# Optimization experiments

Measured on AMD Instinct MI355X. Metric: run time of the kernel, lower is better.

Reference implementation:

```python
import jax, jax.numpy as jnp
import numpy as np

GDEP = 3
BETA = 0.05
C_IN = 32
C_OUT = 64
N_NODES = 512
B = 8
SEQ = 256


def setup_inputs() -> dict:
    key = jax.random.key(0)
    k1, k2, k3, k4 = jax.random.split(key, 4)
    X = jax.random.normal(k1, (B, C_IN, N_NODES, SEQ), dtype=jnp.float32)
    A = jax.random.uniform(k2, (N_NODES, N_NODES), dtype=jnp.float32)
    # 1x1 conv over channels: weight [c_out, (gdep+1)*c_in], bias [c_out]
    fan_in = (GDEP + 1) * C_IN
    limit = float(np.sqrt(6.0 / (C_OUT + fan_in)))  # xavier_uniform
    W = jax.random.uniform(k3, (C_OUT, fan_in), minval=-limit, maxval=limit, dtype=jnp.float32)
    b = jax.random.uniform(k4, (C_OUT,), dtype=jnp.float32)
    return {"X": X, "A": A, "W": W, "b": b}


def reference(X, A, W, b):
    # A <- row-normalized (A + I)
    n = A.shape[0]
    A = A + jnp.eye(n, dtype=A.dtype)
    A = A / jnp.sum(A, axis=1, keepdims=True)
    H = X
    hops = [X]
    for _ in range(GDEP):
        # Hk[n,c,v,l] = sum_w H[n,c,w,l] * A[v,w]
        Hk = jnp.einsum('ncwl,vw->ncvl', H, A)
        H = BETA * X + (1.0 - BETA) * Hk
        hops.append(H)
    H0 = jnp.concatenate(hops, axis=1)  # [B, (gdep+1)*c_in, N, L]
    # 1x1 conv == channel matmul
    out = jnp.einsum('bcnl,oc->bonl', H0, W) + b[None, :, None, None]
    return out
```

## Files before the change

kernel.cpp:

```cpp
#include <hip/hip_runtime.h>


#define NODES 512
#define SEQL  256
#define CIN   32
#define COUT  64
#define NB    8
#define PLANE (NODES * SEQL)
#define BETA_F 0.05f

typedef _Float16 f16x8 __attribute__((ext_vector_type(8)));
typedef _Float16 f16x2 __attribute__((ext_vector_type(2)));
typedef float    f32x4 __attribute__((ext_vector_type(4)));

typedef const unsigned int __attribute__((address_space(1)))* gptr_t;
typedef unsigned int __attribute__((address_space(3)))* lptr_t;

__device__ __forceinline__ void gload16(const void* g, void* l) {
    __builtin_amdgcn_global_load_lds((gptr_t)g, (lptr_t)l, 16, 0, 0);
}

__device__ __forceinline__ unsigned short f2h(float f) {
    _Float16 h = (_Float16)f;
    return __builtin_bit_cast(unsigned short, h);
}

__global__ __launch_bounds__(256) void norm_A_kernel(const float* __restrict__ A,
                                                     _Float16* __restrict__ Apb) {
    const int v = blockIdx.x;
    const int t = threadIdx.x;
    __shared__ float red[256];
    float s = 0.f;
    for (int w = t; w < NODES; w += 256)
        s += A[v * NODES + w] + (w == v ? 1.f : 0.f);
    red[t] = s;
    __syncthreads();
    for (int off = 128; off > 0; off >>= 1) {
        if (t < off) red[t] += red[t + off];
        __syncthreads();
    }
    const float inv = (1.f - BETA_F) / red[0];
    for (int w = t; w < NODES; w += 256) {
        const float a = A[v * NODES + w] + (w == v ? 1.f : 0.f);
        Apb[v * NODES + w] = (_Float16)(a * inv);
    }
}

__global__ __launch_bounds__(256) void prep_W_kernel(const float* __restrict__ W,
                                                     float* __restrict__ Wt,
                                                     unsigned int* __restrict__ Wp) {
    const int i = blockIdx.x * 256 + threadIdx.x;
    const int o = i >> 7, c = i & 127;
    Wt[c * COUT + o] = W[i];
    if (i < 4096) {
        const int p = i >> 6, oo = i & 63;
        Wp[i] = (unsigned)f2h(W[oo * 128 + 2 * p]) |
                ((unsigned)f2h(W[oo * 128 + 2 * p + 1]) << 16);
    }
}

__global__ __launch_bounds__(256) void prep_X_kernel(const float* __restrict__ X,
                                                     unsigned short* __restrict__ Xt) {
    const int l0 = blockIdx.x * 64, v0 = blockIdx.y * 64;
    const size_t coff = (size_t)blockIdx.z * PLANE;
    __shared__ unsigned short t[64][66];
    const int rr = threadIdx.x >> 4;
    const int cc = (threadIdx.x & 15) * 4;
#pragma unroll
    for (int rep = 0; rep < 4; ++rep) {
        const int vl = rep * 16 + rr;
        const float4 f = *(const float4*)(X + coff + (size_t)(v0 + vl) * SEQL + l0 + cc);
        t[cc + 0][vl] = f2h(f.x);
        t[cc + 1][vl] = f2h(f.y);
        t[cc + 2][vl] = f2h(f.z);
        t[cc + 3][vl] = f2h(f.w);
    }
    __syncthreads();
#pragma unroll
    for (int rep = 0; rep < 4; ++rep) {
        const int ll = rep * 16 + rr;
        ushort4 d;
        d.x = t[ll][cc + 0]; d.y = t[ll][cc + 1];
        d.z = t[ll][cc + 2]; d.w = t[ll][cc + 3];
        *(ushort4*)(Xt + coff + (size_t)(l0 + ll) * NODES + v0 + cc) = d;
    }
}

__global__ __launch_bounds__(256) void transpose_h_kernel(const unsigned short* __restrict__ src,
                                                          unsigned short* __restrict__ dst) {
    const int v0 = blockIdx.x * 64, l0 = blockIdx.y * 64;
    const size_t coff = (size_t)blockIdx.z * PLANE;
    __shared__ unsigned short t[64][66];
    const int rr = threadIdx.x >> 4;
    const int cc = (threadIdx.x & 15) * 4;
#pragma unroll
    for (int rep = 0; rep < 4; ++rep) {
        const int ll = rep * 16 + rr;
        const ushort4 s = *(const ushort4*)(src + coff + (size_t)(l0 + ll) * NODES + v0 + cc);
        t[cc + 0][ll] = s.x; t[cc + 1][ll] = s.y;
        t[cc + 2][ll] = s.z; t[cc + 3][ll] = s.w;
    }
    __syncthreads();
#pragma unroll
    for (int rep = 0; rep < 4; ++rep) {
        const int vl = rep * 16 + rr;
        ushort4 d;
        d.x = t[vl][cc + 0]; d.y = t[vl][cc + 1];
        d.z = t[vl][cc + 2]; d.w = t[vl][cc + 3];
        *(ushort4*)(dst + coff + (size_t)(v0 + vl) * SEQL + l0 + cc) = d;
    }
}

__global__ __launch_bounds__(256) void prop_mfma_kernel(
    const _Float16* __restrict__ Apb,
    const _Float16* __restrict__ Hin,
    const _Float16* __restrict__ Xt,
    _Float16* __restrict__ Hout)
{
    __shared__ _Float16 Asl[128 * 64];
    __shared__ _Float16 Bsl[128 * 64];

    const int tid  = threadIdx.x;
    const int wave = tid >> 6;
    const int lane = tid & 63;
    const int n0 = blockIdx.x * 128;
    const int m0 = blockIdx.y * 128;
    const size_t coff = (size_t)blockIdx.z * PLANE;
    const _Float16* Asrc = Hin + coff;

    const int wm = (wave >> 1) * 64;
    const int wn = (wave & 1) * 64;
    const int lane15 = lane & 15;
    const int quad = lane >> 4;
    const int srow = lane >> 3;
    const int spos = lane & 7;

    f32x4 acc[4][4] = {};

    for (int kk = 0; kk < 8; ++kk) {
        const int k0 = kk * 64;
#pragma unroll
        for (int j = 0; j < 4; ++j) {
            const int r = wave * 32 + j * 8 + srow;
            const int gc = k0 + ((spos ^ (r & 7)) << 3);
            gload16(Asrc + (size_t)(m0 + r) * NODES + gc, &Asl[(wave * 32 + j * 8) * 64]);
            gload16(Apb  + (size_t)(n0 + r) * NODES + gc, &Bsl[(wave * 32 + j * 8) * 64]);
        }
        __syncthreads();
#pragma unroll
        for (int ks = 0; ks < 2; ++ks) {
            f16x8 af[4], bf[4];
#pragma unroll
            for (int mt = 0; mt < 4; ++mt) {
                const int m = wm + mt * 16 + lane15;
                const int pos = (ks * 4 + quad) ^ (m & 7);
                af[mt] = *(const f16x8*)&Asl[m * 64 + pos * 8];
            }
#pragma unroll
            for (int nt = 0; nt < 4; ++nt) {
                const int n = wn + nt * 16 + lane15;
                const int pos = (ks * 4 + quad) ^ (n & 7);
                bf[nt] = *(const f16x8*)&Bsl[n * 64 + pos * 8];
            }
#pragma unroll
            for (int mt = 0; mt < 4; ++mt)
#pragma unroll
                for (int nt = 0; nt < 4; ++nt)
                    acc[mt][nt] = __builtin_amdgcn_mfma_f32_16x16x32_f16(
                        af[mt], bf[nt], acc[mt][nt], 0, 0, 0);
        }
        __syncthreads();
    }

#pragma unroll
    for (int mt = 0; mt < 4; ++mt) {
#pragma unroll
        for (int nt = 0; nt < 4; ++nt) {
            const int l = m0 + wm + mt * 16 + quad * 4;
            const int v = n0 + wn + nt * 16 + lane15;
            const size_t base = coff + (size_t)l * NODES + v;
#pragma unroll
            for (int r = 0; r < 4; ++r) {
                const size_t a = base + (size_t)r * NODES;
                Hout[a] = (_Float16)(acc[mt][nt][r] + BETA_F * (float)Xt[a]);
            }
        }
    }
}

__global__ __launch_bounds__(256) void final_kernel(
    const float* __restrict__ X,
    const _Float16* __restrict__ H1,
    const _Float16* __restrict__ H2,
    const _Float16* __restrict__ H3,
    const float* __restrict__ Wt,
    const unsigned int* __restrict__ Wp,
    const float* __restrict__ bias,
    float* __restrict__ out)
{
    const int v = blockIdx.x, b = blockIdx.y, l = threadIdx.x;
    const size_t vl = (size_t)v * SEQL + l;

    float acc[COUT];
#pragma unroll
    for (int o = 0; o < COUT; ++o) acc[o] = bias[o];

    {
        const float* P = X + (size_t)b * CIN * PLANE + vl;
        for (int c = 0; c < CIN; ++c) {
            const float x = P[(size_t)c * PLANE];
            const float* wr = Wt + c * COUT;
#pragma unroll
            for (int o = 0; o < COUT; ++o) acc[o] += wr[o] * x;
        }
    }
    const _Float16* Hs[3] = {H1, H2, H3};
#pragma unroll
    for (int g = 0; g < 3; ++g) {
        const _Float16* P = Hs[g] + (size_t)b * CIN * PLANE + vl;
        for (int cp = 0; cp < 16; ++cp) {
            const _Float16 h0 = P[(size_t)(2 * cp) * PLANE];
            const _Float16 h1 = P[(size_t)(2 * cp + 1) * PLANE];
            const f16x2 hp = {h0, h1};
            const unsigned int* wr = Wp + ((g + 1) * 16 + cp) * COUT;
#pragma unroll
            for (int o = 0; o < COUT; ++o)
                acc[o] = __builtin_amdgcn_fdot2(hp, __builtin_bit_cast(f16x2, wr[o]),
                                                acc[o], false);
        }
    }
    float* O = out + (size_t)b * COUT * PLANE + vl;
#pragma unroll
    for (int o = 0; o < COUT; ++o) O[(size_t)o * PLANE] = acc[o];
}

extern "C" void kernel_launch(void* const* d_in, const int* in_sizes, int n_in,
                              void* d_out, int out_size, void* d_ws, size_t ws_size,
                              hipStream_t stream) {
    (void)in_sizes; (void)n_in; (void)out_size; (void)ws_size;
    const float* X    = (const float*)d_in[0];
    const float* A    = (const float*)d_in[1];
    const float* W    = (const float*)d_in[2];
    const float* bias = (const float*)d_in[3];
    float* out = (float*)d_out;
    char* w = (char*)d_ws;

    const size_t MB = 1ull << 20;
    float*          Wt  = (float*)(w);
    unsigned int*   Wp  = (unsigned int*)(w + 64 * 1024);
    _Float16*       Apb = (_Float16*)(w + 128 * 1024);
    _Float16*       Xt  = (_Float16*)(w + 1 * MB);
    _Float16*       Ht1 = (_Float16*)(w + 65 * MB);
    _Float16*       Ht2 = (_Float16*)(w + 129 * MB);
    _Float16*       Ht3 = (_Float16*)(w + 193 * MB);
    _Float16*       Hn1 = (_Float16*)(w + 257 * MB);
    _Float16*       Hn2 = (_Float16*)(w + 321 * MB);
    _Float16*       Hn3 = (_Float16*)(w + 385 * MB);

    norm_A_kernel<<<dim3(NODES), dim3(256), 0, stream>>>(A, Apb);
    prep_W_kernel<<<dim3(32), dim3(256), 0, stream>>>(W, Wt, Wp);
    prep_X_kernel<<<dim3(4, 8, 256), dim3(256), 0, stream>>>(X, (unsigned short*)Xt);

    const dim3 pgrid(4, 2, 256);
    const dim3 tgrid(8, 4, 256);

    prop_mfma_kernel<<<pgrid, 256, 0, stream>>>(Apb, Xt, Xt, Ht1);
    transpose_h_kernel<<<tgrid, 256, 0, stream>>>((const unsigned short*)Ht1, (unsigned short*)Hn1);
    prop_mfma_kernel<<<pgrid, 256, 0, stream>>>(Apb, Ht1, Xt, Ht2);
    transpose_h_kernel<<<tgrid, 256, 0, stream>>>((const unsigned short*)Ht2, (unsigned short*)Hn2);
    prop_mfma_kernel<<<pgrid, 256, 0, stream>>>(Apb, Ht2, Xt, Ht3);
    transpose_h_kernel<<<tgrid, 256, 0, stream>>>((const unsigned short*)Ht3, (unsigned short*)Hn3);

    final_kernel<<<dim3(NODES, NB), dim3(256), 0, stream>>>(X, Hn1, Hn2, Hn3, Wt, Wp, bias, out);
}
```

Before: 799.2 us.

## Precompute hop propagation matrices and apply all hops in one batched GEMM

The propagation is linear, so each hop can be written as H_k = M_k X with M_1 = P + βI and M_{k+1} = M_k P + βI. The change builds these three small 512x512 matrices with two tiny GEMMs, then computes all three hops straight from X in a single batched MFMA kernel that writes output already in node-major layout. This removes the three dependent large propagation passes and the three transpose kernels, allowing all hops to run concurrently. Per-element FLOPs stay the same, and fp16 rounding now builds up in M_k instead of in H.

```diff
diff --git a/kernel.cpp b/kernel.cpp
--- a/kernel.cpp
+++ b/kernel.cpp
@@ -26,7 +26,8 @@
 }
 
 __global__ __launch_bounds__(256) void norm_A_kernel(const float* __restrict__ A,
-                                                     _Float16* __restrict__ Apb) {
+                                                     _Float16* __restrict__ M1,
+                                                     _Float16* __restrict__ Pt) {
     const int v = blockIdx.x;
     const int t = threadIdx.x;
     __shared__ float red[256];
@@ -41,8 +42,9 @@
     }
     const float inv = (1.f - BETA_F) / red[0];
     for (int w = t; w < NODES; w += 256) {
-        const float a = A[v * NODES + w] + (w == v ? 1.f : 0.f);
-        Apb[v * NODES + w] = (_Float16)(a * inv);
+        const float p = (A[v * NODES + w] + (w == v ? 1.f : 0.f)) * inv;
+        M1[v * NODES + w] = (_Float16)(p + (w == v ? BETA_F : 0.f));
+        Pt[w * NODES + v] = (_Float16)p;
     }
 }
 
@@ -86,36 +88,10 @@
     }
 }
 
-__global__ __launch_bounds__(256) void transpose_h_kernel(const unsigned short* __restrict__ src,
-                                                          unsigned short* __restrict__ dst) {
-    const int v0 = blockIdx.x * 64, l0 = blockIdx.y * 64;
-    const size_t coff = (size_t)blockIdx.z * PLANE;
-    __shared__ unsigned short t[64][66];
-    const int rr = threadIdx.x >> 4;
-    const int cc = (threadIdx.x & 15) * 4;
-#pragma unroll
-    for (int rep = 0; rep < 4; ++rep) {
-        const int ll = rep * 16 + rr;
-        const ushort4 s = *(const ushort4*)(src + coff + (size_t)(l0 + ll) * NODES + v0 + cc);
-        t[cc + 0][ll] = s.x; t[cc + 1][ll] = s.y;
-        t[cc + 2][ll] = s.z; t[cc + 3][ll] = s.w;
-    }
-    __syncthreads();
-#pragma unroll
-    for (int rep = 0; rep < 4; ++rep) {
-        const int vl = rep * 16 + rr;
-        ushort4 d;
-        d.x = t[vl][cc + 0]; d.y = t[vl][cc + 1];
-        d.z = t[vl][cc + 2]; d.w = t[vl][cc + 3];
-        *(ushort4*)(dst + coff + (size_t)(v0 + vl) * SEQL + l0 + cc) = d;
-    }
-}
-
-__global__ __launch_bounds__(256) void prop_mfma_kernel(
-    const _Float16* __restrict__ Apb,
-    const _Float16* __restrict__ Hin,
-    const _Float16* __restrict__ Xt,
-    _Float16* __restrict__ Hout)
+__global__ __launch_bounds__(256) void small_mm_kernel(
+    const _Float16* __restrict__ Min,
+    const _Float16* __restrict__ Pt,
+    _Float16* __restrict__ Mout)
 {
     __shared__ _Float16 Asl[128 * 64];
     __shared__ _Float16 Bsl[128 * 64];
@@ -125,8 +101,6 @@
     const int lane = tid & 63;
     const int n0 = blockIdx.x * 128;
     const int m0 = blockIdx.y * 128;
-    const size_t coff = (size_t)blockIdx.z * PLANE;
-    const _Float16* Asrc = Hin + coff;
 
     const int wm = (wave >> 1) * 64;
     const int wn = (wave & 1) * 64;
@@ -143,8 +117,8 @@
         for (int j = 0; j < 4; ++j) {
             const int r = wave * 32 + j * 8 + srow;
             const int gc = k0 + ((spos ^ (r & 7)) << 3);
-            gload16(Asrc + (size_t)(m0 + r) * NODES + gc, &Asl[(wave * 32 + j * 8) * 64]);
-            gload16(Apb  + (size_t)(n0 + r) * NODES + gc, &Bsl[(wave * 32 + j * 8) * 64]);
+            gload16(Min + (size_t)(m0 + r) * NODES + gc, &Asl[(wave * 32 + j * 8) * 64]);
+            gload16(Pt  + (size_t)(n0 + r) * NODES + gc, &Bsl[(wave * 32 + j * 8) * 64]);
         }
         __syncthreads();
 #pragma unroll
@@ -176,14 +150,96 @@
     for (int mt = 0; mt < 4; ++mt) {
 #pragma unroll
         for (int nt = 0; nt < 4; ++nt) {
-            const int l = m0 + wm + mt * 16 + quad * 4;
-            const int v = n0 + wn + nt * 16 + lane15;
-            const size_t base = coff + (size_t)l * NODES + v;
-#pragma unroll
-            for (int r = 0; r < 4; ++r) {
-                const size_t a = base + (size_t)r * NODES;
-                Hout[a] = (_Float16)(acc[mt][nt][r] + BETA_F * (float)Xt[a]);
+            const int v = m0 + wm + mt * 16 + quad * 4;
+            const int w = n0 + wn + nt * 16 + lane15;
+#pragma unroll
+            for (int r = 0; r < 4; ++r)
+                Mout[(size_t)(v + r) * NODES + w] =
+                    (_Float16)(acc[mt][nt][r] + ((v + r) == w ? BETA_F : 0.f));
+        }
+    }
+}
+
+__global__ __launch_bounds__(256) void hop_mfma_kernel(
+    const _Float16* __restrict__ M1,
+    const _Float16* __restrict__ M2,
+    const _Float16* __restrict__ M3,
+    const _Float16* __restrict__ Xt,
+    _Float16* __restrict__ H1,
+    _Float16* __restrict__ H2,
+    _Float16* __restrict__ H3)
+{
+    __shared__ _Float16 Asl[128 * 64];
+    __shared__ _Float16 Bsl[128 * 64];
+
+    const int z = blockIdx.z;
+    const int chunk = z / 3;
+    const int g = z - 3 * chunk;
+    const _Float16* __restrict__ M = (g == 0) ? M1 : (g == 1) ? M2 : M3;
+    _Float16* __restrict__ H = (g == 0) ? H1 : (g == 1) ? H2 : H3;
+
+    const int tid  = threadIdx.x;
+    const int wave = tid >> 6;
+    const int lane = tid & 63;
+    const int n0 = blockIdx.x * 128;
+    const int m0 = blockIdx.y * 128;
+    const size_t coff = (size_t)chunk * PLANE;
+    const _Float16* Bsrc = Xt + coff;
+
+    const int wm = (wave >> 1) * 64;
+    const int wn = (wave & 1) * 64;
+    const int lane15 = lane & 15;
+    const int quad = lane >> 4;
+    const int srow = lane >> 3;
+    const int spos = lane & 7;
+
+    f32x4 acc[4][4] = {};
+
+    for (int kk = 0; kk < 8; ++kk) {
+        const int k0 = kk * 64;
+#pragma unroll
+        for (int j = 0; j < 4; ++j) {
+            const int r = wave * 32 + j * 8 + srow;
+            const int gc = k0 + ((spos ^ (r & 7)) << 3);
+            gload16(M    + (size_t)(m0 + r) * NODES + gc, &Asl[(wave * 32 + j * 8) * 64]);
+            gload16(Bsrc + (size_t)(n0 + r) * NODES + gc, &Bsl[(wave * 32 + j * 8) * 64]);
+        }
+        __syncthreads();
+#pragma unroll
+        for (int ks = 0; ks < 2; ++ks) {
+            f16x8 af[4], bf[4];
+#pragma unroll
+            for (int mt = 0; mt < 4; ++mt) {
+                const int m = wm + mt * 16 + lane15;
+                const int pos = (ks * 4 + quad) ^ (m & 7);
+                af[mt] = *(const f16x8*)&Asl[m * 64 + pos * 8];
             }
+#pragma unroll
+            for (int nt = 0; nt < 4; ++nt) {
+                const int n = wn + nt * 16 + lane15;
+                const int pos = (ks * 4 + quad) ^ (n & 7);
+                bf[nt] = *(const f16x8*)&Bsl[n * 64 + pos * 8];
+            }
+#pragma unroll
+            for (int mt = 0; mt < 4; ++mt)
+#pragma unroll
+                for (int nt = 0; nt < 4; ++nt)
+                    acc[mt][nt] = __builtin_amdgcn_mfma_f32_16x16x32_f16(
+                        af[mt], bf[nt], acc[mt][nt], 0, 0, 0);
+        }
+        __syncthreads();
+    }
+
+#pragma unroll
+    for (int mt = 0; mt < 4; ++mt) {
+#pragma unroll
+        for (int nt = 0; nt < 4; ++nt) {
+            const int v = m0 + wm + mt * 16 + quad * 4;
+            const int l = n0 + wn + nt * 16 + lane15;
+            const size_t base = coff + (size_t)v * SEQL + l;
+#pragma unroll
+            for (int r = 0; r < 4; ++r)
+                H[base + (size_t)r * SEQL] = (_Float16)acc[mt][nt][r];
         }
     }
 }
@@ -246,30 +302,26 @@
     char* w = (char*)d_ws;
 
     const size_t MB = 1ull << 20;
-    float*          Wt  = (float*)(w);
-    unsigned int*   Wp  = (unsigned int*)(w + 64 * 1024);
-    _Float16*       Apb = (_Float16*)(w + 128 * 1024);
-    _Float16*       Xt  = (_Float16*)(w + 1 * MB);
-    _Float16*       Ht1 = (_Float16*)(w + 65 * MB);
-    _Float16*       Ht2 = (_Float16*)(w + 129 * MB);
-    _Float16*       Ht3 = (_Float16*)(w + 193 * MB);
-    _Float16*       Hn1 = (_Float16*)(w + 257 * MB);
-    _Float16*       Hn2 = (_Float16*)(w + 321 * MB);
-    _Float16*       Hn3 = (_Float16*)(w + 385 * MB);
-
-    norm_A_kernel<<<dim3(NODES), dim3(256), 0, stream>>>(A, Apb);
+    float*        Wt  = (float*)(w);
+    unsigned int* Wp  = (unsigned int*)(w + 64 * 1024);
+    _Float16*     M1  = (_Float16*)(w + 1 * MB);
+    _Float16*     M2  = (_Float16*)(w + 2 * MB);
+    _Float16*     M3  = (_Float16*)(w + 3 * MB);
+    _Float16*     Pt  = (_Float16*)(w + 4 * MB);
+    _Float16*     Xt  = (_Float16*)(w + 16 * MB);
+    _Float16*     Hn1 = (_Float16*)(w + 80 * MB);
+    _Float16*     Hn2 = (_Float16*)(w + 144 * MB);
+    _Float16*     Hn3 = (_Float16*)(w + 208 * MB);
+
+    norm_A_kernel<<<dim3(NODES), dim3(256), 0, stream>>>(A, M1, Pt);
     prep_W_kernel<<<dim3(32), dim3(256), 0, stream>>>(W, Wt, Wp);
     prep_X_kernel<<<dim3(4, 8, 256), dim3(256), 0, stream>>>(X, (unsigned short*)Xt);
 
-    const dim3 pgrid(4, 2, 256);
-    const dim3 tgrid(8, 4, 256);
-
-    prop_mfma_kernel<<<pgrid, 256, 0, stream>>>(Apb, Xt, Xt, Ht1);
-    transpose_h_kernel<<<tgrid, 256, 0, stream>>>((const unsigned short*)Ht1, (unsigned short*)Hn1);
-    prop_mfma_kernel<<<pgrid, 256, 0, stream>>>(Apb, Ht1, Xt, Ht2);
-    transpose_h_kernel<<<tgrid, 256, 0, stream>>>((const unsigned short*)Ht2, (unsigned short*)Hn2);
-    prop_mfma_kernel<<<pgrid, 256, 0, stream>>>(Apb, Ht2, Xt, Ht3);
-    transpose_h_kernel<<<tgrid, 256, 0, stream>>>((const unsigned short*)Ht3, (unsigned short*)Hn3);
+    small_mm_kernel<<<dim3(4, 4), dim3(256), 0, stream>>>(M1, Pt, M2);
+    small_mm_kernel<<<dim3(4, 4), dim3(256), 0, stream>>>(M2, Pt, M3);
+
+    hop_mfma_kernel<<<dim3(2, 4, 768), dim3(256), 0, stream>>>(
+        M1, M2, M3, Xt, Hn1, Hn2, Hn3);
 
     final_kernel<<<dim3(NODES, NB), dim3(256), 0, stream>>>(X, Hn1, Hn2, Hn3, Wt, Wp, bias, out);
 }
```

New measurement: 707.9 us. 1.13x faster.
